# Performance work log

Measured on AMD Instinct MI355X. Metric: run time of the kernel, lower is better.

Reference implementation:

```python
import jax, jax.numpy as jnp
import numpy as np

B, N, M, K = 1024, 20000, 10000, 8
CHK_W, OBS_W = 8, 200          # fixed support size per check / observable row
EPS = 1e-6
BETA = 0.5


def setup_inputs() -> dict:
    rng = np.random.default_rng(0)
    # packed CSR-style support sets (fixed row weight -> dense index tables)
    chk_cols = jnp.asarray(rng.integers(0, N, size=(M, CHK_W)), dtype=jnp.int32)
    obs_cols = jnp.asarray(rng.integers(0, N, size=(K, OBS_W)), dtype=jnp.int32)
    key = jax.random.key(0)
    k1, k2, k3 = jax.random.split(key, 3)
    llrs = jax.random.normal(k1, (B, N), dtype=jnp.float32) * 2.0
    syndromes = jax.random.bernoulli(k2, 0.5, (B, M)).astype(jnp.float32)
    observables = jax.random.bernoulli(k3, 0.5, (B, K)).astype(jnp.float32)
    return {"llrs": llrs, "syndromes": syndromes, "observables": observables,
            "chk_cols": chk_cols, "obs_cols": obs_cols}


def _pred_llr(tanh_half, cols):
    # tanh_half: (B, N); cols: (R, W) -> gathered (B, R, W)
    g = tanh_half[:, cols]
    prod = jnp.prod(g, axis=-1)                       # BP check-node tanh product, (B, R)
    prod = jnp.clip(prod, -1.0 + EPS, 1.0 - EPS)
    return 2.0 * jnp.arctanh(prod)


def _bce_with_logits(z, y):
    # BCEWithLogitsLoss(z, y) = softplus(z) - z*y (numerically stable)
    return jax.nn.softplus(z) - z * y


def reference(llrs, syndromes, observables, chk_cols, obs_cols):
    t = jnp.tanh(llrs * 0.5)                          # (B, N)
    syn_pred_llr = _pred_llr(t, chk_cols)             # (B, M)
    obs_pred_llr = _pred_llr(t, obs_cols)             # (B, K)
    loss1 = _bce_with_logits(-syn_pred_llr, syndromes).sum(axis=1)
    loss2 = _bce_with_logits(-obs_pred_llr, observables).sum(axis=1)
    loss = BETA * loss1 + (1.0 - BETA) * loss2
    return loss.mean()
```

## Files before the change

### kernel.cpp

```cpp
#include <hip/hip_runtime.h>

#define B_ 1024
#define N_ 20000
#define M_ 10000
#define K_ 8
#define OBS_W_ 200
#define TPB 1024
#define NV4 (N_ / 4)

constexpr float EPS_   = 1e-6f;
constexpr float LN2_   = 0.69314718055994530942f;
constexpr float LOG2E_ = 1.4426950408889634f;

typedef _Float16 f16x2 __attribute__((ext_vector_type(2)));
typedef _Float16 f16x8 __attribute__((ext_vector_type(8)));

__device__ __forceinline__ float tanh_half_fast(float x) {
    float e = __builtin_amdgcn_exp2f(x * LOG2E_);
    return 1.0f - 2.0f * __builtin_amdgcn_rcpf(e + 1.0f);
}

__device__ __forceinline__ float bce_log2(float p, float y) {
    p = fminf(fmaxf(p, -1.0f + EPS_), 1.0f - EPS_);
    float w = fmaf(1.0f - 2.0f * y, p, 1.0f);
    return __builtin_amdgcn_logf(w);
}

__device__ __forceinline__ void do_check2(const f16x2* __restrict__ t2,
                                          const float* __restrict__ synA,
                                          const float* __restrict__ synB,
                                          const int4* __restrict__ cc,
                                          int m, float& acc, int& nterm) {
    int4 c0 = cc[2 * m];
    int4 c1 = cc[2 * m + 1];
    f16x2 g0 = t2[c0.x], g1 = t2[c0.y], g2 = t2[c0.z], g3 = t2[c0.w];
    f16x2 g4 = t2[c1.x], g5 = t2[c1.y], g6 = t2[c1.z], g7 = t2[c1.w];
    f16x2 p  = ((g0 * g1) * (g2 * g3)) * ((g4 * g5) * (g6 * g7));
    acc += bce_log2((float)p[0], synA[m]);
    acc += bce_log2((float)p[1], synB[m]);
    nterm += 2;
}

__device__ __forceinline__ f16x8 pack2(float4 a, float4 c) {
    f16x8 v;
    v[0] = (_Float16)tanh_half_fast(a.x); v[1] = (_Float16)tanh_half_fast(c.x);
    v[2] = (_Float16)tanh_half_fast(a.y); v[3] = (_Float16)tanh_half_fast(c.y);
    v[4] = (_Float16)tanh_half_fast(a.z); v[5] = (_Float16)tanh_half_fast(c.z);
    v[6] = (_Float16)tanh_half_fast(a.w); v[7] = (_Float16)tanh_half_fast(c.w);
    return v;
}

template <bool ATOMIC>
__global__ __launch_bounds__(TPB) void decode_loss_pipe(
    const float* __restrict__ llrs,
    const float* __restrict__ syndromes,
    const float* __restrict__ observables,
    const int*   __restrict__ chk_cols,
    const int*   __restrict__ obs_cols,
    float* __restrict__ part)
{
    extern __shared__ char smem_raw[];
    f16x2* t2a = reinterpret_cast<f16x2*>(smem_raw);
    f16x2* t2b = t2a + N_;
    __shared__ float red[TPB / 64];

    const int b0  = 4 * blockIdx.x;
    const int tid = threadIdx.x;

    const float4* r0 = reinterpret_cast<const float4*>(llrs + (size_t)(b0 + 0) * N_);
    const float4* r1 = reinterpret_cast<const float4*>(llrs + (size_t)(b0 + 1) * N_);
    const float4* r2 = reinterpret_cast<const float4*>(llrs + (size_t)(b0 + 2) * N_);
    const float4* r3 = reinterpret_cast<const float4*>(llrs + (size_t)(b0 + 3) * N_);

    for (int i = tid; i < NV4; i += TPB) {
        *reinterpret_cast<f16x8*>(&t2a[4 * i]) = pack2(r0[i], r1[i]);
    }
    __syncthreads();

    const float* syn0 = syndromes + (size_t)(b0 + 0) * M_;
    const float* syn1 = syndromes + (size_t)(b0 + 1) * M_;
    const float* syn2 = syndromes + (size_t)(b0 + 2) * M_;
    const float* syn3 = syndromes + (size_t)(b0 + 3) * M_;
    const int4*  cc   = reinterpret_cast<const int4*>(chk_cols);

    float acc   = 0.0f;
    int   nterm = 0;

    #pragma unroll 1
    for (int it = 0; it < 5; ++it) {
        const int  i  = tid + it * TPB;
        const bool iv = (i < NV4);
        float4 a, c;
        if (iv) { a = r2[i]; c = r3[i]; }
        const int m0 = tid + (2 * it) * TPB;
        const int m1 = m0 + TPB;
        if (m0 < M_) do_check2(t2a, syn0, syn1, cc, m0, acc, nterm);
        if (m1 < M_) do_check2(t2a, syn0, syn1, cc, m1, acc, nterm);
        if (iv) *reinterpret_cast<f16x8*>(&t2b[4 * i]) = pack2(a, c);
    }
    __syncthreads();

    for (int m = tid; m < M_; m += TPB) {
        do_check2(t2b, syn2, syn3, cc, m, acc, nterm);
    }

    float sum = 0.5f * LN2_ * ((float)nterm - acc);

    if (tid < 256) {
        const int row  = tid >> 6;
        const int k    = (tid >> 3) & 7;
        const int seg  = tid & 7;
        const f16x2* tb   = (row < 2) ? t2a : t2b;
        const int    comp = row & 1;
        const int*   oc   = obs_cols + k * OBS_W_ + seg * 25;
        float pr = 1.0f;
        #pragma unroll 5
        for (int w = 0; w < 25; ++w) pr *= (float)tb[oc[w]][comp];
        #pragma unroll
        for (int off = 1; off < 8; off <<= 1) pr *= __shfl_xor(pr, off, 64);
        if (seg == 0) {
            float y = observables[(size_t)(b0 + row) * K_ + k];
            sum += 0.5f * LN2_ * (1.0f - bce_log2(pr, y));
        }
    }

    for (int off = 32; off > 0; off >>= 1) sum += __shfl_down(sum, off, 64);
    const int lane = tid & 63, wv = tid >> 6;
    if (lane == 0) red[wv] = sum;
    __syncthreads();
    if (tid == 0) {
        float tot = 0.0f;
        #pragma unroll
        for (int i = 0; i < TPB / 64; ++i) tot += red[i];
        if (ATOMIC) atomicAdd(part, tot * (1.0f / (float)B_));
        else        part[blockIdx.x] = tot;
    }
}

__global__ __launch_bounds__(256) void decode_loss_reduce(
    const float* __restrict__ part, float* __restrict__ out, int n)
{
    __shared__ float red[4];
    const int tid = threadIdx.x;
    float s = 0.0f;
    for (int i = tid; i < n; i += 256) s += part[i];
    for (int off = 32; off > 0; off >>= 1) s += __shfl_down(s, off, 64);
    const int lane = tid & 63, wv = tid >> 6;
    if (lane == 0) red[wv] = s;
    __syncthreads();
    if (tid == 0) out[0] = (red[0] + red[1] + red[2] + red[3]) * (1.0f / (float)B_);
}

extern "C" void kernel_launch(void* const* d_in, const int* in_sizes, int n_in,
                              void* d_out, int out_size, void* d_ws, size_t ws_size,
                              hipStream_t stream) {
    const float* llrs        = (const float*)d_in[0];
    const float* syndromes   = (const float*)d_in[1];
    const float* observables = (const float*)d_in[2];
    const int*   chk_cols    = (const int*)d_in[3];
    const int*   obs_cols    = (const int*)d_in[4];
    float*       out         = (float*)d_out;

    const size_t lds_bytes = (size_t)N_ * 2 * sizeof(f16x2);
    const int    nblk      = B_ / 4;

    (void)hipFuncSetAttribute((const void*)decode_loss_pipe<false>,
        hipFuncAttributeMaxDynamicSharedMemorySize, (int)lds_bytes);
    (void)hipFuncSetAttribute((const void*)decode_loss_pipe<true>,
        hipFuncAttributeMaxDynamicSharedMemorySize, (int)lds_bytes);

    if (ws_size >= (size_t)nblk * sizeof(float)) {
        float* part = (float*)d_ws;
        decode_loss_pipe<false><<<nblk, TPB, lds_bytes, stream>>>(
            llrs, syndromes, observables, chk_cols, obs_cols, part);
        decode_loss_reduce<<<1, 256, 0, stream>>>(part, out, nblk);
    } else {
        hipMemsetAsync(out, 0, sizeof(float), stream);
        decode_loss_pipe<true><<<nblk, TPB, lds_bytes, stream>>>(
            llrs, syndromes, observables, chk_cols, obs_cols, out);
    }
}
```

Before: 29.23 us.

## Prefetch second row pair into registers upfront and merge log calls via products

All llr loads for rows 2-3 are now issued into registers before the first check pass, and their conversion into the second LDS buffer is moved after that pass, so the global-load latency overlaps the whole first pass. Check loops are fully unrolled. Each thread now multiplies the two per-check (1 ± p) factors across two checks and takes one log per four terms, which cuts transcendental work. The costs are higher register pressure at 1024 threads per block (ten float4 held live), possible spills, and a small precision risk from multiplying several factors before the log.

```diff
diff --git a/kernel.cpp b/kernel.cpp
--- a/kernel.cpp
+++ b/kernel.cpp
@@ -7,6 +7,8 @@
 #define OBS_W_ 200
 #define TPB 1024
 #define NV4 (N_ / 4)
+#define NLOAD 5
+#define NCHK 10
 
 constexpr float EPS_   = 1e-6f;
 constexpr float LN2_   = 0.69314718055994530942f;
@@ -20,25 +22,24 @@
     return 1.0f - 2.0f * __builtin_amdgcn_rcpf(e + 1.0f);
 }
 
-__device__ __forceinline__ float bce_log2(float p, float y) {
-    p = fminf(fmaxf(p, -1.0f + EPS_), 1.0f - EPS_);
-    float w = fmaf(1.0f - 2.0f * y, p, 1.0f);
-    return __builtin_amdgcn_logf(w);
-}
-
-__device__ __forceinline__ void do_check2(const f16x2* __restrict__ t2,
-                                          const float* __restrict__ synA,
-                                          const float* __restrict__ synB,
-                                          const int4* __restrict__ cc,
-                                          int m, float& acc, int& nterm) {
+__device__ __forceinline__ float clampp(float p) {
+    return fminf(fmaxf(p, -1.0f + EPS_), 1.0f - EPS_);
+}
+
+__device__ __forceinline__ float wprod2(const f16x2* __restrict__ t2,
+                                        const float* __restrict__ synA,
+                                        const float* __restrict__ synB,
+                                        const int4* __restrict__ cc, int m) {
     int4 c0 = cc[2 * m];
     int4 c1 = cc[2 * m + 1];
     f16x2 g0 = t2[c0.x], g1 = t2[c0.y], g2 = t2[c0.z], g3 = t2[c0.w];
     f16x2 g4 = t2[c1.x], g5 = t2[c1.y], g6 = t2[c1.z], g7 = t2[c1.w];
     f16x2 p  = ((g0 * g1) * (g2 * g3)) * ((g4 * g5) * (g6 * g7));
-    acc += bce_log2((float)p[0], synA[m]);
-    acc += bce_log2((float)p[1], synB[m]);
-    nterm += 2;
+    float pa = clampp((float)p[0]);
+    float pb = clampp((float)p[1]);
+    float w0 = fmaf(fmaf(synA[m], -2.0f, 1.0f), pa, 1.0f);
+    float w1 = fmaf(fmaf(synB[m], -2.0f, 1.0f), pb, 1.0f);
+    return w0 * w1;
 }
 
 __device__ __forceinline__ f16x8 pack2(float4 a, float4 c) {
@@ -51,7 +52,7 @@
 }
 
 template <bool ATOMIC>
-__global__ __launch_bounds__(TPB) void decode_loss_pipe(
+__global__ __launch_bounds__(TPB) void decode_loss_dp(
     const float* __restrict__ llrs,
     const float* __restrict__ syndromes,
     const float* __restrict__ observables,
@@ -77,6 +78,13 @@
     }
     __syncthreads();
 
+    float4 pa[NLOAD], pc[NLOAD];
+    #pragma unroll
+    for (int s = 0; s < NLOAD; ++s) {
+        const int i = tid + s * TPB;
+        if (i < NV4) { pa[s] = r2[i]; pc[s] = r3[i]; }
+    }
+
     const float* syn0 = syndromes + (size_t)(b0 + 0) * M_;
     const float* syn1 = syndromes + (size_t)(b0 + 1) * M_;
     const float* syn2 = syndromes + (size_t)(b0 + 2) * M_;
@@ -86,22 +94,35 @@
     float acc   = 0.0f;
     int   nterm = 0;
 
-    #pragma unroll 1
-    for (int it = 0; it < 5; ++it) {
-        const int  i  = tid + it * TPB;
-        const bool iv = (i < NV4);
-        float4 a, c;
-        if (iv) { a = r2[i]; c = r3[i]; }
-        const int m0 = tid + (2 * it) * TPB;
+    #pragma unroll
+    for (int it = 0; it < NCHK; it += 2) {
+        const int m0 = tid + it * TPB;
         const int m1 = m0 + TPB;
-        if (m0 < M_) do_check2(t2a, syn0, syn1, cc, m0, acc, nterm);
-        if (m1 < M_) do_check2(t2a, syn0, syn1, cc, m1, acc, nterm);
-        if (iv) *reinterpret_cast<f16x8*>(&t2b[4 * i]) = pack2(a, c);
-    }
-    __syncthreads();
-
-    for (int m = tid; m < M_; m += TPB) {
-        do_check2(t2b, syn2, syn3, cc, m, acc, nterm);
+        float w = 1.0f;
+        int   c = 0;
+        if (m0 < M_) { w *= wprod2(t2a, syn0, syn1, cc, m0); c += 2; }
+        if (m1 < M_) { w *= wprod2(t2a, syn0, syn1, cc, m1); c += 2; }
+        acc += __builtin_amdgcn_logf(w);
+        nterm += c;
+    }
+
+    #pragma unroll
+    for (int s = 0; s < NLOAD; ++s) {
+        const int i = tid + s * TPB;
+        if (i < NV4) *reinterpret_cast<f16x8*>(&t2b[4 * i]) = pack2(pa[s], pc[s]);
+    }
+    __syncthreads();
+
+    #pragma unroll
+    for (int it = 0; it < NCHK; it += 2) {
+        const int m0 = tid + it * TPB;
+        const int m1 = m0 + TPB;
+        float w = 1.0f;
+        int   c = 0;
+        if (m0 < M_) { w *= wprod2(t2b, syn2, syn3, cc, m0); c += 2; }
+        if (m1 < M_) { w *= wprod2(t2b, syn2, syn3, cc, m1); c += 2; }
+        acc += __builtin_amdgcn_logf(w);
+        nterm += c;
     }
 
     float sum = 0.5f * LN2_ * ((float)nterm - acc);
@@ -119,8 +140,10 @@
         #pragma unroll
         for (int off = 1; off < 8; off <<= 1) pr *= __shfl_xor(pr, off, 64);
         if (seg == 0) {
-            float y = observables[(size_t)(b0 + row) * K_ + k];
-            sum += 0.5f * LN2_ * (1.0f - bce_log2(pr, y));
+            float y  = observables[(size_t)(b0 + row) * K_ + k];
+            float p  = clampp(pr);
+            float w2 = fmaf(fmaf(y, -2.0f, 1.0f), p, 1.0f);
+            sum += 0.5f * LN2_ * (1.0f - __builtin_amdgcn_logf(w2));
         }
     }
 
@@ -164,19 +187,19 @@
     const size_t lds_bytes = (size_t)N_ * 2 * sizeof(f16x2);
     const int    nblk      = B_ / 4;
 
-    (void)hipFuncSetAttribute((const void*)decode_loss_pipe<false>,
+    (void)hipFuncSetAttribute((const void*)decode_loss_dp<false>,
         hipFuncAttributeMaxDynamicSharedMemorySize, (int)lds_bytes);
-    (void)hipFuncSetAttribute((const void*)decode_loss_pipe<true>,
+    (void)hipFuncSetAttribute((const void*)decode_loss_dp<true>,
         hipFuncAttributeMaxDynamicSharedMemorySize, (int)lds_bytes);
 
     if (ws_size >= (size_t)nblk * sizeof(float)) {
         float* part = (float*)d_ws;
-        decode_loss_pipe<false><<<nblk, TPB, lds_bytes, stream>>>(
+        decode_loss_dp<false><<<nblk, TPB, lds_bytes, stream>>>(
             llrs, syndromes, observables, chk_cols, obs_cols, part);
         decode_loss_reduce<<<1, 256, 0, stream>>>(part, out, nblk);
     } else {
         hipMemsetAsync(out, 0, sizeof(float), stream);
-        decode_loss_pipe<true><<<nblk, TPB, lds_bytes, stream>>>(
+        decode_loss_dp<true><<<nblk, TPB, lds_bytes, stream>>>(
             llrs, syndromes, observables, chk_cols, obs_cols, out);
     }
 }
```

New measurement: 43.83 us. 50.0% more time.
